# Optimization experiments

Measured on AMD Instinct MI355X. Metric: run time of the kernel, lower is better.

Reference implementation:

```python
import jax, jax.numpy as jnp
import numpy as np

B, C, H, W = 1, 8192, 32, 32
C8 = C // 8  # 1024 == H*W; required by the (b,hw,hw)/(b,c8) broadcast in the original code


def setup_inputs() -> dict:
    key = jax.random.key(0)
    ks = jax.random.split(key, 11)
    rn = lambda i, shape, s=1.0: jax.random.normal(ks[i], shape, dtype=jnp.float32) * s
    return {
        "x": rn(0, (B, C, H, W)),
        "Wq": rn(1, (C8, C), 0.02),
        "Wk": rn(2, (C8, C), 0.02),
        "Wv": rn(3, (C, C), 0.02),
        "q_scale": jax.random.uniform(ks[4], (C8,), minval=0.5, maxval=1.5),
        "q_shift": rn(5, (C8,), 0.1),
        "k_scale": jax.random.uniform(ks[6], (C8,), minval=0.5, maxval=1.5),
        "k_shift": rn(7, (C8,), 0.1),
        "v_scale": jax.random.uniform(ks[8], (C,), minval=0.5, maxval=1.5),
        "v_shift": rn(9, (C,), 0.1),
        "gamma": rn(10, (), 0.5),
    }


def reference(x, Wq, Wk, Wv, q_scale, q_shift, k_scale, k_shift, v_scale, v_shift, gamma):
    b, c, h, w = x.shape
    n = h * w
    xf = x.reshape(b, c, n)  # (b, c, n)
    # BasicConv2d = 1x1 conv (no bias) + BatchNorm2d; BN folded to per-channel scale/shift
    q = jnp.einsum('oc,bcn->bon', Wq, xf) * q_scale[:, None] + q_shift[:, None]  # (b, c8, n)
    k = jnp.einsum('oc,bcn->bon', Wk, xf) * k_scale[:, None] + k_shift[:, None]  # (b, c8, n)
    v = jnp.einsum('oc,bcn->bon', Wv, xf) * v_scale[:, None] + v_shift[:, None]  # (b, c,  n)
    q = q.transpose(0, 2, 1)  # (b, n, c8)
    # PPMCC score: per-channel centering, covariance across channels
    q_c = q - q.mean(axis=1, keepdims=True)
    k_c = k - k.mean(axis=2, keepdims=True)
    cov = jnp.einsum('bnc,bcm->bnm', q_c, k_c) / (n - 1)  # (b, n, n)
    q_std = q.std(axis=1)  # (b, c8), ddof=0 (matches torch unbiased=False)
    k_std = k.std(axis=2)  # (b, c8)
    ppmcc = cov / (q_std * k_std)  # broadcasts over last axis since c8 == n
    att = jax.nn.softmax(ppmcc, axis=-1).transpose(0, 2, 1)  # (b, n, n)
    out = jnp.einsum('bcn,bnm->bcm', v, att).reshape(b, c, h, w)
    return gamma * out + x
```

## Files before the change

### kernel.cpp

```cpp
#include <hip/hip_runtime.h>
#include <cstdint>
#include <cstddef>

#define CDIM 8192
#define NDIM 1024
#define C8D  1024
#define MSTACK 10240
#define NT8 128

typedef __bf16 bf16_t;
typedef __bf16 bf16x8 __attribute__((ext_vector_type(8)));
typedef __bf16 bf16x4 __attribute__((ext_vector_type(4)));
typedef float  f32x4  __attribute__((ext_vector_type(4)));

__device__ __forceinline__ void gload_lds16(const void* g, void* l) {
    __builtin_amdgcn_global_load_lds((const __attribute__((address_space(1))) void*)g,
                                     (__attribute__((address_space(3))) void*)l, 16, 0, 0);
}

__global__ __launch_bounds__(256) void cvt_bf16_k(const float* __restrict__ in,
                                                  bf16_t* __restrict__ out, int n8) {
    int idx = blockIdx.x * 256 + threadIdx.x;
    int stride = gridDim.x * 256;
    for (int i = idx; i < n8; i += stride) {
        size_t off = (size_t)i * 8;
        float4 a = *(const float4*)(in + off);
        float4 b = *(const float4*)(in + off + 4);
        bf16x8 o = { (__bf16)a.x, (__bf16)a.y, (__bf16)a.z, (__bf16)a.w,
                     (__bf16)b.x, (__bf16)b.y, (__bf16)b.z, (__bf16)b.w };
        *(bf16x8*)(out + off) = o;
    }
}

__global__ __launch_bounds__(256) void transpose_cvt_x(const float* __restrict__ x,
                                                       bf16_t* __restrict__ xT) {
    __shared__ float t[32][33];
    const int n0 = blockIdx.x * 32, c0 = blockIdx.y * 32;
    const int tx = threadIdx.x, ty = threadIdx.y;
    #pragma unroll
    for (int i = 0; i < 4; ++i)
        t[ty + i * 8][tx] = x[(size_t)(c0 + ty + i * 8) * NDIM + n0 + tx];
    __syncthreads();
    #pragma unroll
    for (int i = 0; i < 4; ++i)
        xT[(size_t)(n0 + ty + i * 8) * CDIM + c0 + tx] = (__bf16)t[tx][ty + i * 8];
}

__global__ __launch_bounds__(512, 2) void mega_gemm8(
    const bf16_t* __restrict__ Wv, const bf16_t* __restrict__ Wq,
    const bf16_t* __restrict__ Wk, const bf16_t* __restrict__ Bx,
    bf16_t* __restrict__ v_out, float* __restrict__ q_out, float* __restrict__ k_out,
    const float* __restrict__ v_scale, const float* __restrict__ v_shift,
    const float* __restrict__ q_scale, const float* __restrict__ q_shift,
    const float* __restrict__ k_scale, const float* __restrict__ k_shift)
{
    __shared__ __align__(16) bf16_t Ld[65536];

    const int tid  = threadIdx.x;
    const int lane = tid & 63;
    const int wid  = tid >> 6;
    const int wr   = wid >> 2;
    const int wc   = wid & 3;

    const int lin  = blockIdx.y * 4 + blockIdx.x;
    const int tile = (lin & 7) * 20 + (lin >> 3);
    const int trow = tile >> 2;
    const int col0 = (tile & 3) * 256;

    const bf16_t* Ag; const float* s0; const float* s1; int arow, path;
    if (trow < 32)      { Ag = Wv; arow = trow * 256;        s0 = v_scale; s1 = v_shift; path = 0; }
    else if (trow < 36) { Ag = Wq; arow = trow * 256 - 8192; s0 = q_scale; s1 = q_shift; path = 1; }
    else                { Ag = Wk; arow = trow * 256 - 9216; s0 = k_scale; s1 = k_shift; path = 2; }

    const int ar0 = tid >> 3;
    const int o0  = tid * 8;
    const int csw = (((tid & 7) ^ ((tid >> 3) & 7)) << 3);

    const int aRow = (wr * 128 + (lane & 15)) * 64;
    const int bRow = 32768 + (wc * 64 + (lane & 15)) * 64;
    const int ac0  = (((lane >> 4) * 8)     ) ^ ((lane & 7) << 3);
    const int ac1  = (32 + ((lane >> 4) * 8)) ^ ((lane & 7) << 3);

    f32x4 acc[8][4];
    #pragma unroll
    for (int mi = 0; mi < 8; ++mi)
        #pragma unroll
        for (int ni = 0; ni < 4; ++ni)
            acc[mi][ni] = (f32x4){0.f, 0.f, 0.f, 0.f};

#define STAGE8(BUF, KB) do {                                                                  \
    gload_lds16(Ag + (size_t)(arow + ar0      ) * CDIM + (KB) + csw, Ld + (BUF)*16384 + o0          ); \
    gload_lds16(Ag + (size_t)(arow + ar0 +  64) * CDIM + (KB) + csw, Ld + (BUF)*16384 + o0 +  4096  ); \
    gload_lds16(Ag + (size_t)(arow + ar0 + 128) * CDIM + (KB) + csw, Ld + (BUF)*16384 + o0 +  8192  ); \
    gload_lds16(Ag + (size_t)(arow + ar0 + 192) * CDIM + (KB) + csw, Ld + (BUF)*16384 + o0 + 12288  ); \
    gload_lds16(Bx + (size_t)(col0 + ar0      ) * CDIM + (KB) + csw, Ld + 32768 + (BUF)*16384 + o0          ); \
    gload_lds16(Bx + (size_t)(col0 + ar0 +  64) * CDIM + (KB) + csw, Ld + 32768 + (BUF)*16384 + o0 +  4096  ); \
    gload_lds16(Bx + (size_t)(col0 + ar0 + 128) * CDIM + (KB) + csw, Ld + 32768 + (BUF)*16384 + o0 +  8192  ); \
    gload_lds16(Bx + (size_t)(col0 + ar0 + 192) * CDIM + (KB) + csw, Ld + 32768 + (BUF)*16384 + o0 + 12288  ); \
} while (0)

#define HALF_MMA(BUF, AC) do {                                                                \
    bf16x8 av[8], bv[4];                                                                      \
    _Pragma("unroll") for (int mi = 0; mi < 8; ++mi)                                          \
        av[mi] = *(const bf16x8*)(Ld + (BUF)*16384 + aRow + mi*1024 + (AC));                  \
    _Pragma("unroll") for (int ni = 0; ni < 4; ++ni)                                          \
        bv[ni] = *(const bf16x8*)(Ld + (BUF)*16384 + bRow + ni*1024 + (AC));                  \
    __builtin_amdgcn_s_setprio(1);                                                            \
    _Pragma("unroll") for (int mi = 0; mi < 8; ++mi)                                          \
        _Pragma("unroll") for (int ni = 0; ni < 4; ++ni)                                      \
            acc[mi][ni] = __builtin_amdgcn_mfma_f32_16x16x32_bf16(av[mi], bv[ni],             \
                                                                  acc[mi][ni], 0, 0, 0);      \
    __builtin_amdgcn_s_setprio(0);                                                            \
} while (0)

#define TILE8(BUF, T) do {                                                                    \
    HALF_MMA(BUF, ac0);                                                                       \
    HALF_MMA(BUF, ac1);                                                                       \
    if ((T) != NT8 - 1) {                                                                     \
        asm volatile("s_waitcnt lgkmcnt(0)" ::: "memory");                                    \
        __builtin_amdgcn_sched_barrier(0);                                                    \
        __builtin_amdgcn_s_barrier();                       \
        __builtin_amdgcn_sched_barrier(0);                                                    \
        if ((T) + 2 < NT8) {                                                                  \
            STAGE8(BUF, ((T) + 2) * 64);                                                      \
            asm volatile("s_waitcnt vmcnt(8)" ::: "memory");                                  \
        } else {                                                                              \
            asm volatile("s_waitcnt vmcnt(0)" ::: "memory");                                  \
        }                                                                                     \
        __builtin_amdgcn_sched_barrier(0);                                                    \
        __builtin_amdgcn_s_barrier();                          \
        __builtin_amdgcn_sched_barrier(0);                                                    \
    }                                                                                         \
} while (0)

    STAGE8(0, 0);
    STAGE8(1, 64);
    asm volatile("s_waitcnt vmcnt(8)" ::: "memory");
    __builtin_amdgcn_sched_barrier(0);
    __builtin_amdgcn_s_barrier();
    __builtin_amdgcn_sched_barrier(0);

    for (int t = 0; t < NT8; t += 2) {
        TILE8(0, t);
        TILE8(1, t + 1);
    }
#undef TILE8
#undef HALF_MMA
#undef STAGE8

    const int cq = (lane >> 4) * 4;
    #pragma unroll
    for (int mi = 0; mi < 8; ++mi) {
        #pragma unroll
        for (int ni = 0; ni < 4; ++ni) {
            const int j = col0 + wc * 64 + ni * 16 + (lane & 15);
            #pragma unroll
            for (int r = 0; r < 4; ++r) {
                const int il = arow + wr * 128 + mi * 16 + cq + r;
                float vv = acc[mi][ni][r] * s0[il] + s1[il];
                if (path == 0)      v_out[(size_t)il * NDIM + j] = (__bf16)vv;
                else if (path == 1) q_out[(size_t)il * NDIM + j] = vv;
                else                k_out[(size_t)il * NDIM + j] = vv;
            }
        }
    }
}

template <int EPI, typename OutT>
__global__ __launch_bounds__(256) void gemm_bt(
    const bf16_t* __restrict__ A, const bf16_t* __restrict__ B,
    OutT* __restrict__ C, int M, int N, int K,
    const float* __restrict__ e0, const float* __restrict__ e1,
    const float* __restrict__ gs)
{
    const int gx = gridDim.x;
    const int nwg = gx * gridDim.y;
    const int lin = blockIdx.y * gx + blockIdx.x;
    int tile = lin;
    if ((nwg & 7) == 0) tile = (lin & 7) * (nwg >> 3) + (lin >> 3);
    const int row0 = (tile / gx) * 128;
    const int col0 = (tile % gx) * 128;

    const int Ks  = K / gridDim.z;
    const int kb0 = blockIdx.z * Ks;
    const int kb1 = kb0 + Ks;
    OutT* Cz = C + (size_t)blockIdx.z * M * N;

    const int tid = threadIdx.x;
    __shared__ __align__(16) bf16_t As[2 * 4096];
    __shared__ __align__(16) bf16_t Bs[2 * 4096];

    const int lane = tid & 63;
    const int w    = tid >> 6;
    const int wm   = (w >> 1) * 64;
    const int wn   = (w & 1) * 64;
    const int lr   = lane & 15;
    const int kg   = (lane >> 4) * 8;

    f32x4 acc[4][4];
    #pragma unroll
    for (int a_ = 0; a_ < 4; ++a_)
        #pragma unroll
        for (int b_ = 0; b_ < 4; ++b_)
            acc[a_][b_] = (f32x4){0.f, 0.f, 0.f, 0.f};

    const int eA = tid * 8;
    const int eB = (256 + tid) * 8;
    const int rA = eA >> 5, cA = eA & 31;
    const int rB = eB >> 5, cB = eB & 31;

#define BT_STAGE(buf, kb)                                                       \
    do {                                                                        \
        gload_lds16(A + (size_t)(row0 + rA) * K + (kb) + cA, As + (buf)*4096 + eA); \
        gload_lds16(A + (size_t)(row0 + rB) * K + (kb) + cB, As + (buf)*4096 + eB); \
        gload_lds16(B + (size_t)(col0 + rA) * K + (kb) + cA, Bs + (buf)*4096 + eA); \
        gload_lds16(B + (size_t)(col0 + rB) * K + (kb) + cB, Bs + (buf)*4096 + eB); \
    } while (0)

    BT_STAGE(0, kb0);
    __syncthreads();
    int cur = 0;
    for (int kb = kb0; kb < kb1; kb += 32) {
        if (kb + 32 < kb1) BT_STAGE(cur ^ 1, kb + 32);
        const bf16_t* Ac = As + cur * 4096;
        const bf16_t* Bc = Bs + cur * 4096;

        bf16x8 av[4], bv[4];
        #pragma unroll
        for (int mi = 0; mi < 4; ++mi)
            av[mi] = *(const bf16x8*)(Ac + (wm + mi * 16 + lr) * 32 + kg);
        #pragma unroll
        for (int ni = 0; ni < 4; ++ni)
            bv[ni] = *(const bf16x8*)(Bc + (wn + ni * 16 + lr) * 32 + kg);

        #pragma unroll
        for (int mi = 0; mi < 4; ++mi)
            #pragma unroll
            for (int ni = 0; ni < 4; ++ni)
                acc[mi][ni] = __builtin_amdgcn_mfma_f32_16x16x32_bf16(
                    av[mi], bv[ni], acc[mi][ni], 0, 0, 0);
        __syncthreads();
        cur ^= 1;
    }
#undef BT_STAGE

    float g = 0.f;
    if (EPI == 3) g = gs[0];
    const int cr = (lane >> 4) * 4;
    #pragma unroll
    for (int mi = 0; mi < 4; ++mi) {
        #pragma unroll
        for (int ni = 0; ni < 4; ++ni) {
            const int j = col0 + wn + ni * 16 + lr;
            float s0 = 0.f, s1 = 0.f;
            if (EPI == 2) { s0 = e0[j]; s1 = e1[j]; }
            #pragma unroll
            for (int r = 0; r < 4; ++r) {
                const int i = row0 + wm + mi * 16 + cr + r;
                float v = acc[mi][ni][r];
                if (EPI == 2)      v = v * (1.0f / 1023.0f) / (s0 * s1);
                else if (EPI == 3) v = g * v + e0[(size_t)i * N + j];
                Cz[(size_t)i * N + j] = (OutT)v;
            }
        }
    }
}

__global__ __launch_bounds__(256) void rowstats(
    const float* __restrict__ Q, const float* __restrict__ Km,
    float* __restrict__ qmean, float* __restrict__ qstd,
    float* __restrict__ kmean, float* __restrict__ kstd)
{
    const int wid  = blockIdx.x * 4 + (threadIdx.x >> 6);
    const int lane = threadIdx.x & 63;
    const float* src = (wid < 1024) ? (Q + (size_t)wid * NDIM)
                                    : (Km + (size_t)(wid - 1024) * NDIM);
    float s = 0.f, s2 = 0.f;
    #pragma unroll
    for (int p = 0; p < 4; ++p) {
        float4 v = *(const float4*)(src + p * 256 + lane * 4);
        s  += v.x + v.y + v.z + v.w;
        s2 += v.x * v.x + v.y * v.y + v.z * v.z + v.w * v.w;
    }
    #pragma unroll
    for (int o = 32; o; o >>= 1) { s += __shfl_xor(s, o); s2 += __shfl_xor(s2, o); }
    if (lane == 0) {
        float m   = s / 1024.f;
        float var = fmaxf(s2 / 1024.f - m * m, 0.f);
        if (wid < 1024) { qmean[wid] = m; qstd[wid] = sqrtf(var); }
        else            { kmean[wid - 1024] = m; kstd[wid - 1024] = sqrtf(var); }
    }
}

__global__ __launch_bounds__(256) void center_tr(
    const float* __restrict__ Q, const float* __restrict__ qmu, bf16_t* __restrict__ qc,
    const float* __restrict__ Km, const float* __restrict__ kmu, bf16_t* __restrict__ kc)
{
    __shared__ float t[32][33];
    const float* M  = blockIdx.z ? Km  : Q;
    const float* mu = blockIdx.z ? kmu : qmu;
    bf16_t* O       = blockIdx.z ? kc  : qc;
    const int o0 = blockIdx.y * 32, n0 = blockIdx.x * 32;
    const int tx = threadIdx.x, ty = threadIdx.y;
    #pragma unroll
    for (int i = 0; i < 4; ++i) {
        const int o = o0 + ty + i * 8;
        t[ty + i * 8][tx] = M[(size_t)o * NDIM + n0 + tx] - mu[o];
    }
    __syncthreads();
    #pragma unroll
    for (int i = 0; i < 4; ++i)
        O[(size_t)(n0 + ty + i * 8) * C8D + o0 + tx] = (__bf16)t[tx][ty + i * 8];
}

__global__ __launch_bounds__(256) void softmax_rows(const float* __restrict__ P,
                                                    bf16_t* __restrict__ O) {
    const int row = blockIdx.x;
    const int tid = threadIdx.x;
    const size_t PL = (size_t)NDIM * NDIM / 4;
    const size_t u  = (size_t)row * (NDIM / 4) + tid;
    const float4* B = (const float4*)P;
    float4 p0 = B[u], p1 = B[u + PL], p2 = B[u + 2 * PL], p3 = B[u + 3 * PL];
    float4 v = { p0.x + p1.x + p2.x + p3.x, p0.y + p1.y + p2.y + p3.y,
                 p0.z + p1.z + p2.z + p3.z, p0.w + p1.w + p2.w + p3.w };
    float mx = fmaxf(fmaxf(v.x, v.y), fmaxf(v.z, v.w));
    #pragma unroll
    for (int o = 32; o; o >>= 1) mx = fmaxf(mx, __shfl_xor(mx, o));
    __shared__ float red[8];
    const int w = tid >> 6, lane = tid & 63;
    if (lane == 0) red[w] = mx;
    __syncthreads();
    mx = fmaxf(fmaxf(red[0], red[1]), fmaxf(red[2], red[3]));
    float e0 = __expf(v.x - mx), e1 = __expf(v.y - mx);
    float e2 = __expf(v.z - mx), e3 = __expf(v.w - mx);
    float s = e0 + e1 + e2 + e3;
    #pragma unroll
    for (int o = 32; o; o >>= 1) s += __shfl_xor(s, o);
    if (lane == 0) red[4 + w] = s;
    __syncthreads();
    s = red[4] + red[5] + red[6] + red[7];
    const float inv = 1.0f / s;
    bf16x4 o4 = { (__bf16)(e0 * inv), (__bf16)(e1 * inv),
                  (__bf16)(e2 * inv), (__bf16)(e3 * inv) };
    ((bf16x4*)(O + (size_t)row * NDIM))[tid] = o4;
}

extern "C" void kernel_launch(void* const* d_in, const int* in_sizes, int n_in,
                              void* d_out, int out_size, void* d_ws, size_t ws_size,
                              hipStream_t stream)
{
    const float* x       = (const float*)d_in[0];
    const float* Wq      = (const float*)d_in[1];
    const float* Wk      = (const float*)d_in[2];
    const float* Wv      = (const float*)d_in[3];
    const float* q_scale = (const float*)d_in[4];
    const float* q_shift = (const float*)d_in[5];
    const float* k_scale = (const float*)d_in[6];
    const float* k_shift = (const float*)d_in[7];
    const float* v_scale = (const float*)d_in[8];
    const float* v_shift = (const float*)d_in[9];
    const float* gamma   = (const float*)d_in[10];
    float* out = (float*)d_out;

    char* w = (char*)d_ws;
    bf16_t* Wv_b = (bf16_t*)w; w += (size_t)CDIM * CDIM * 2;
    bf16_t* Wq_b = (bf16_t*)w; w += (size_t)C8D  * CDIM * 2;
    bf16_t* Wk_b = (bf16_t*)w; w += (size_t)C8D  * CDIM * 2;
    bf16_t* xT   = (bf16_t*)w; w += (size_t)NDIM * CDIM * 2;
    bf16_t* v_b  = (bf16_t*)w; w += (size_t)CDIM * NDIM * 2;
    float*  q_on = (float*) w; w += (size_t)C8D * NDIM * 4;
    float*  k_on = (float*) w; w += (size_t)C8D * NDIM * 4;
    float*  P    = (float*) w; w += (size_t)4 * NDIM * NDIM * 4;
    bf16_t* qc   = (bf16_t*)w; w += (size_t)NDIM * C8D * 2;
    bf16_t* kc   = (bf16_t*)w; w += (size_t)NDIM * C8D * 2;
    bf16_t* A0   = (bf16_t*)w; w += (size_t)NDIM * NDIM * 2;
    float*  qmean = (float*)w; w += C8D * 4;
    float*  qstd  = (float*)w; w += C8D * 4;
    float*  kmean = (float*)w; w += C8D * 4;
    float*  kstd  = (float*)w; w += C8D * 4;

    cvt_bf16_k<<<2048, 256, 0, stream>>>(Wv, Wv_b, (int)((size_t)CDIM * CDIM / 8));
    cvt_bf16_k<<<2048, 256, 0, stream>>>(Wq, Wq_b, C8D * CDIM / 8);
    cvt_bf16_k<<<2048, 256, 0, stream>>>(Wk, Wk_b, C8D * CDIM / 8);
    transpose_cvt_x<<<dim3(NDIM / 32, CDIM / 32), dim3(32, 8), 0, stream>>>(x, xT);

    mega_gemm8<<<dim3(4, MSTACK / 256), 512, 0, stream>>>(
        Wv_b, Wq_b, Wk_b, xT, v_b, q_on, k_on,
        v_scale, v_shift, q_scale, q_shift, k_scale, k_shift);

    rowstats<<<512, 256, 0, stream>>>(q_on, k_on, qmean, qstd, kmean, kstd);

    center_tr<<<dim3(32, 32, 2), dim3(32, 8), 0, stream>>>(
        q_on, qmean, qc, k_on, kmean, kc);

    gemm_bt<2, float><<<dim3(NDIM / 128, NDIM / 128, 4), 256, 0, stream>>>(
        qc, kc, P, NDIM, NDIM, C8D, qstd, kstd, nullptr);

    softmax_rows<<<NDIM, 256, 0, stream>>>(P, A0);

    gemm_bt<3, float><<<dim3(NDIM / 128, CDIM / 128, 1), 256, 0, stream>>>(
        v_b, A0, out, CDIM, NDIM, NDIM, x, x, gamma);
}
```

Baseline: 416.4 us.

## Split projection GEMM K-tile into quadrant phases interleaving loads with MFMA

Restructures the main projection GEMM's inner loop into four quadrant phases per K-tile. Each 256x256 tile is split into 128x128 halves, and each phase issues one half-stage of global-to-LDS prefetch, reads only the fragments it needs and runs a smaller MFMA block. The goal is to spread memory issue and LDS reads across the compute so that load latency overlaps MFMA work better, in the style of ping-pong scheduling. In exchange it adds more barriers per K-tile, and the vmcnt bookkeeping becomes fragile, since some A-half prefetches write into the buffer currently being read.

```diff
diff --git a/kernel.cpp b/kernel.cpp
--- a/kernel.cpp
+++ b/kernel.cpp
@@ -76,91 +76,141 @@
     const int o0  = tid * 8;
     const int csw = (((tid & 7) ^ ((tid >> 3) & 7)) << 3);
 
-    const int aRow = (wr * 128 + (lane & 15)) * 64;
-    const int bRow = 32768 + (wc * 64 + (lane & 15)) * 64;
-    const int ac0  = (((lane >> 4) * 8)     ) ^ ((lane & 7) << 3);
-    const int ac1  = (32 + ((lane >> 4) * 8)) ^ ((lane & 7) << 3);
-
-    f32x4 acc[8][4];
-    #pragma unroll
-    for (int mi = 0; mi < 8; ++mi)
-        #pragma unroll
-        for (int ni = 0; ni < 4; ++ni)
-            acc[mi][ni] = (f32x4){0.f, 0.f, 0.f, 0.f};
-
-#define STAGE8(BUF, KB) do {                                                                  \
-    gload_lds16(Ag + (size_t)(arow + ar0      ) * CDIM + (KB) + csw, Ld + (BUF)*16384 + o0          ); \
-    gload_lds16(Ag + (size_t)(arow + ar0 +  64) * CDIM + (KB) + csw, Ld + (BUF)*16384 + o0 +  4096  ); \
-    gload_lds16(Ag + (size_t)(arow + ar0 + 128) * CDIM + (KB) + csw, Ld + (BUF)*16384 + o0 +  8192  ); \
-    gload_lds16(Ag + (size_t)(arow + ar0 + 192) * CDIM + (KB) + csw, Ld + (BUF)*16384 + o0 + 12288  ); \
-    gload_lds16(Bx + (size_t)(col0 + ar0      ) * CDIM + (KB) + csw, Ld + 32768 + (BUF)*16384 + o0          ); \
-    gload_lds16(Bx + (size_t)(col0 + ar0 +  64) * CDIM + (KB) + csw, Ld + 32768 + (BUF)*16384 + o0 +  4096  ); \
-    gload_lds16(Bx + (size_t)(col0 + ar0 + 128) * CDIM + (KB) + csw, Ld + 32768 + (BUF)*16384 + o0 +  8192  ); \
-    gload_lds16(Bx + (size_t)(col0 + ar0 + 192) * CDIM + (KB) + csw, Ld + 32768 + (BUF)*16384 + o0 + 12288  ); \
-} while (0)
-
-#define HALF_MMA(BUF, AC) do {                                                                \
-    bf16x8 av[8], bv[4];                                                                      \
-    _Pragma("unroll") for (int mi = 0; mi < 8; ++mi)                                          \
-        av[mi] = *(const bf16x8*)(Ld + (BUF)*16384 + aRow + mi*1024 + (AC));                  \
-    _Pragma("unroll") for (int ni = 0; ni < 4; ++ni)                                          \
-        bv[ni] = *(const bf16x8*)(Ld + (BUF)*16384 + bRow + ni*1024 + (AC));                  \
+    const int lr   = lane & 15;
+    const int hi8  = (lane >> 4) * 8;
+    const int rsw  = (lane & 7) << 3;
+    const int ck0  = hi8 ^ rsw;
+    const int ck1  = (32 + hi8) ^ rsw;
+    const int aRow = wr * 64 + lr;
+    const int bRow = wc * 32 + lr;
+
+    bf16x8 av[4][2];
+    bf16x8 bv[2][2][2];
+    f32x4  acc[2][2][4][2];
+    #pragma unroll
+    for (int mh = 0; mh < 2; ++mh)
+        #pragma unroll
+        for (int nh = 0; nh < 2; ++nh)
+            #pragma unroll
+            for (int fi = 0; fi < 4; ++fi)
+                #pragma unroll
+                for (int fj = 0; fj < 2; ++fj)
+                    acc[mh][nh][fi][fj] = (f32x4){0.f, 0.f, 0.f, 0.f};
+
+#define STAGE_AH(BUF, H, KB) do {                                                             \
+    gload_lds16(Ag + (size_t)(arow + (H)*128 + ar0     ) * CDIM + (KB) + csw,                 \
+                Ld + (BUF)*16384 + (H)*8192 + o0);                                            \
+    gload_lds16(Ag + (size_t)(arow + (H)*128 + ar0 + 64) * CDIM + (KB) + csw,                 \
+                Ld + (BUF)*16384 + (H)*8192 + o0 + 4096);                                     \
+} while (0)
+
+#define STAGE_BH(BUF, H, KB) do {                                                             \
+    gload_lds16(Bx + (size_t)(col0 + (H)*128 + ar0     ) * CDIM + (KB) + csw,                 \
+                Ld + 32768 + (BUF)*16384 + (H)*8192 + o0);                                    \
+    gload_lds16(Bx + (size_t)(col0 + (H)*128 + ar0 + 64) * CDIM + (KB) + csw,                 \
+                Ld + 32768 + (BUF)*16384 + (H)*8192 + o0 + 4096);                             \
+} while (0)
+
+#define RD_A(BUF, MH) do {                                                                    \
+    _Pragma("unroll") for (int fi = 0; fi < 4; ++fi) {                                        \
+        av[fi][0] = *(const bf16x8*)(Ld + (BUF)*16384 + ((MH)*128 + aRow + fi*16)*64 + ck0);  \
+        av[fi][1] = *(const bf16x8*)(Ld + (BUF)*16384 + ((MH)*128 + aRow + fi*16)*64 + ck1);  \
+    }                                                                                         \
+} while (0)
+
+#define RD_B(BUF, NH) do {                                                                    \
+    _Pragma("unroll") for (int fj = 0; fj < 2; ++fj) {                                        \
+        bv[NH][fj][0] = *(const bf16x8*)(Ld + 32768 + (BUF)*16384 +                           \
+                                         ((NH)*128 + bRow + fj*16)*64 + ck0);                 \
+        bv[NH][fj][1] = *(const bf16x8*)(Ld + 32768 + (BUF)*16384 +                           \
+                                         ((NH)*128 + bRow + fj*16)*64 + ck1);                 \
+    }                                                                                         \
+} while (0)
+
+#define MMA(MH, NH) do {                                                                      \
     __builtin_amdgcn_s_setprio(1);                                                            \
-    _Pragma("unroll") for (int mi = 0; mi < 8; ++mi)                                          \
-        _Pragma("unroll") for (int ni = 0; ni < 4; ++ni)                                      \
-            acc[mi][ni] = __builtin_amdgcn_mfma_f32_16x16x32_bf16(av[mi], bv[ni],             \
-                                                                  acc[mi][ni], 0, 0, 0);      \
+    _Pragma("unroll") for (int kk = 0; kk < 2; ++kk)                                          \
+        _Pragma("unroll") for (int fi = 0; fi < 4; ++fi)                                      \
+            _Pragma("unroll") for (int fj = 0; fj < 2; ++fj)                                  \
+                acc[MH][NH][fi][fj] = __builtin_amdgcn_mfma_f32_16x16x32_bf16(                \
+                    av[fi][kk], bv[NH][fj][kk], acc[MH][NH][fi][fj], 0, 0, 0);                \
     __builtin_amdgcn_s_setprio(0);                                                            \
 } while (0)
 
-#define TILE8(BUF, T) do {                                                                    \
-    HALF_MMA(BUF, ac0);                                                                       \
-    HALF_MMA(BUF, ac1);                                                                       \
-    if ((T) != NT8 - 1) {                                                                     \
-        asm volatile("s_waitcnt lgkmcnt(0)" ::: "memory");                                    \
-        __builtin_amdgcn_sched_barrier(0);                                                    \
-        __builtin_amdgcn_s_barrier();                       \
-        __builtin_amdgcn_sched_barrier(0);                                                    \
-        if ((T) + 2 < NT8) {                                                                  \
-            STAGE8(BUF, ((T) + 2) * 64);                                                      \
-            asm volatile("s_waitcnt vmcnt(8)" ::: "memory");                                  \
-        } else {                                                                              \
-            asm volatile("s_waitcnt vmcnt(0)" ::: "memory");                                  \
-        }                                                                                     \
-        __builtin_amdgcn_sched_barrier(0);                                                    \
-        __builtin_amdgcn_s_barrier();                          \
-        __builtin_amdgcn_sched_barrier(0);                                                    \
-    }                                                                                         \
-} while (0)
-
-    STAGE8(0, 0);
-    STAGE8(1, 64);
-    asm volatile("s_waitcnt vmcnt(8)" ::: "memory");
+#define SYNC_TOP do {                                                                         \
+    __builtin_amdgcn_s_barrier();                                                             \
+    asm volatile("s_waitcnt lgkmcnt(0)" ::: "memory");                                        \
+    __builtin_amdgcn_sched_barrier(0);                                                        \
+} while (0)
+
+#define SYNC_END do {                                                                         \
+    __builtin_amdgcn_s_barrier();                                                             \
+} while (0)
+
+#define KTILE(BUF, T, DO_S2, VM) do {                                                         \
+                                                                          \
+    RD_A(BUF, 0); RD_B(BUF, 0);                                                               \
+    if ((T) + 1 < NT8) STAGE_BH((BUF)^1, 1, ((T)+1)*64);                                      \
+    SYNC_TOP; MMA(0, 0); SYNC_END;                                                            \
+                                                                          \
+    RD_B(BUF, 1);                                                                             \
+    if (DO_S2) STAGE_AH(BUF, 0, ((T)+2)*64);                                                  \
+    SYNC_TOP; MMA(0, 1); SYNC_END;                                                            \
+                                                                          \
+    RD_A(BUF, 1);                                                                             \
+    if (DO_S2) STAGE_BH(BUF, 0, ((T)+2)*64);                                                  \
+    SYNC_TOP; MMA(1, 1); SYNC_END;                                                            \
+                                                         \
+    if (DO_S2) STAGE_AH(BUF, 1, ((T)+2)*64);                                                  \
+    SYNC_TOP; MMA(1, 0);                                                                      \
+    if ((VM) == 6)      { asm volatile("s_waitcnt vmcnt(6)" ::: "memory");                    \
+                          __builtin_amdgcn_sched_barrier(0); }                                \
+    else if ((VM) == 0) { asm volatile("s_waitcnt vmcnt(0)" ::: "memory");                    \
+                          __builtin_amdgcn_sched_barrier(0); }                                \
+    SYNC_END;                                                                                 \
+} while (0)
+
+    STAGE_AH(0, 0, 0); STAGE_BH(0, 0, 0); STAGE_AH(0, 1, 0); STAGE_BH(0, 1, 0);
+    STAGE_AH(1, 0, 64); STAGE_BH(1, 0, 64); STAGE_AH(1, 1, 64);
+    asm volatile("s_waitcnt vmcnt(6)" ::: "memory");
     __builtin_amdgcn_sched_barrier(0);
     __builtin_amdgcn_s_barrier();
-    __builtin_amdgcn_sched_barrier(0);
-
-    for (int t = 0; t < NT8; t += 2) {
-        TILE8(0, t);
-        TILE8(1, t + 1);
-    }
-#undef TILE8
-#undef HALF_MMA
-#undef STAGE8
+
+    for (int t = 0; t < NT8 - 2; t += 2) {
+        KTILE(0, t,     1, 6);
+        KTILE(1, t + 1, 1, 6);
+    }
+    KTILE(0, NT8 - 2, 0, 0);
+    KTILE(1, NT8 - 1, 0, -1);
+
+#undef KTILE
+#undef SYNC_END
+#undef SYNC_TOP
+#undef MMA
+#undef RD_B
+#undef RD_A
+#undef STAGE_BH
+#undef STAGE_AH
 
     const int cq = (lane >> 4) * 4;
     #pragma unroll
-    for (int mi = 0; mi < 8; ++mi) {
-        #pragma unroll
-        for (int ni = 0; ni < 4; ++ni) {
-            const int j = col0 + wc * 64 + ni * 16 + (lane & 15);
+    for (int mh = 0; mh < 2; ++mh) {
+        #pragma unroll
+        for (int nh = 0; nh < 2; ++nh) {
             #pragma unroll
-            for (int r = 0; r < 4; ++r) {
-                const int il = arow + wr * 128 + mi * 16 + cq + r;
-                float vv = acc[mi][ni][r] * s0[il] + s1[il];
-                if (path == 0)      v_out[(size_t)il * NDIM + j] = (__bf16)vv;
-                else if (path == 1) q_out[(size_t)il * NDIM + j] = vv;
-                else                k_out[(size_t)il * NDIM + j] = vv;
+            for (int fi = 0; fi < 4; ++fi) {
+                #pragma unroll
+                for (int fj = 0; fj < 2; ++fj) {
+                    const int j = col0 + nh * 128 + wc * 32 + fj * 16 + lr;
+                    #pragma unroll
+                    for (int r = 0; r < 4; ++r) {
+                        const int il = arow + mh * 128 + wr * 64 + fi * 16 + cq + r;
+                        float vv = acc[mh][nh][fi][fj][r] * s0[il] + s1[il];
+                        if (path == 0)      v_out[(size_t)il * NDIM + j] = (__bf16)vv;
+                        else if (path == 1) q_out[(size_t)il * NDIM + j] = vv;
+                        else                k_out[(size_t)il * NDIM + j] = vv;
+                    }
+                }
             }
         }
     }
```

Result: faster. 355.3 us (-14.7%).
